# Kernel tuning notes

Hardware: AMD Instinct MI355X
Metric: run time of the kernel (lower is better)

## Reference

```python
import jax, jax.numpy as jnp
import numpy as np

B = 4096      # batch
N = 8192      # feature dim (sorted axis)
K_SPARSE = 512


def setup_inputs() -> dict:
    key = jax.random.key(0)
    x = jax.random.normal(key, (B, N), dtype=jnp.float32)
    return {"x": x, "k": K_SPARSE}


def reference(x, k):
    # Train-phase branch of KSparse.call:
    #   kth_smallest = sort(x)[..., N-1-k]  (the (k+1)-th largest value per row)
    #   out = x * (x > kth_smallest[:, None])
    n = x.shape[-1]
    kth = jnp.sort(x, axis=-1)[..., n - 1 - k]          # [B]
    mask = (x > kth[..., None]).astype(x.dtype)          # strictly greater -> keeps top-k
    return x * mask
```

## Files before the change

kernel.cpp:

```cpp
#include <hip/hip_runtime.h>

#define NTHREADS 512
#define N_FEAT   8192
#define EPT      (N_FEAT / NTHREADS)

__device__ __forceinline__ unsigned f2k(float f) {
    unsigned u = __float_as_uint(f);
    return u ^ (unsigned)(((int)u >> 31) | 0x80000000);
}
__device__ __forceinline__ float k2f(unsigned kk) {
    return __uint_as_float(kk ^ (unsigned)(((int)(~kk) >> 31) | 0x80000000));
}

template<int NB, int SHIFT, bool FILTER>
__device__ __forceinline__ void radix_pass(unsigned* hist, const unsigned (&key)[EPT],
                                           unsigned& prefix, unsigned& pmask, unsigned& r,
                                           unsigned* s_pr, int t) {
    constexpr int PER = NB / 64;
    constexpr int L2P = (PER == 64) ? 6 : 4;
    constexpr int PHYS = NB + 64;

#pragma unroll
    for (int i = 0; i < (PHYS + NTHREADS - 1) / NTHREADS; ++i) {
        int idx = t + i * NTHREADS;
        if (idx < PHYS) hist[idx] = 0;
    }
    __syncthreads();

#pragma unroll
    for (int i = 0; i < EPT; ++i) {
        unsigned kk = key[i];
        if (!FILTER || (kk & pmask) == prefix) {
            unsigned b = (kk >> SHIFT) & (NB - 1);
            atomicAdd(&hist[b + (b >> L2P)], 1u);
        }
    }
    __syncthreads();

    if (t < 64) {
        const unsigned* hbase = hist + t * (PER + 1);
        unsigned C = 0;
#pragma unroll
        for (int j = 0; j < PER; ++j) C += hbase[j];
        unsigned S = C;
#pragma unroll
        for (int off = 1; off < 64; off <<= 1) {
            unsigned v = (unsigned)__shfl_down((int)S, off, 64);
            if (t + off < 64) S += v;
        }
        unsigned carry = S - C;
        if (S >= r && carry < r) {
            unsigned acc = carry;
#pragma unroll
            for (int j = PER - 1; j >= 0; --j) {
                unsigned ge = acc + hbase[j];
                if (ge >= r && acc < r) {
                    s_pr[0] = prefix | ((unsigned)(t * PER + j) << SHIFT);
                    s_pr[1] = r - acc;
                }
                acc = ge;
            }
        }
    }
    __syncthreads();
    prefix = s_pr[0];
    r = s_pr[1];
    pmask |= (unsigned)(NB - 1) << SHIFT;
}

__global__ __launch_bounds__(NTHREADS) void ksparse_kernel(
    const float* __restrict__ x, const int* __restrict__ kptr,
    float* __restrict__ out) {
    const int row = blockIdx.x;
    const int t   = threadIdx.x;
    const size_t base = (size_t)row * N_FEAT;

    __shared__ unsigned hist[4096 + 64];
    __shared__ unsigned s_pr[2];

    const float4* xv = (const float4*)(x + base);
    unsigned key[EPT];
#pragma unroll
    for (int i = 0; i < EPT / 4; ++i) {
        float4 v = xv[t + i * NTHREADS];
        key[4 * i + 0] = f2k(v.x);
        key[4 * i + 1] = f2k(v.y);
        key[4 * i + 2] = f2k(v.z);
        key[4 * i + 3] = f2k(v.w);
    }

    unsigned r = (unsigned)kptr[0] + 1u;
    unsigned prefix = 0, pmask = 0;

    radix_pass<4096, 20, false>(hist, key, prefix, pmask, r, s_pr, t);
    radix_pass<1024, 10, true >(hist, key, prefix, pmask, r, s_pr, t);
    radix_pass<1024,  0, true >(hist, key, prefix, pmask, r, s_pr, t);

    const unsigned kth = prefix;
    float4* ov = (float4*)(out + base);
#pragma unroll
    for (int i = 0; i < EPT / 4; ++i) {
        float4 o;
        unsigned k0 = key[4 * i + 0];
        unsigned k1 = key[4 * i + 1];
        unsigned k2 = key[4 * i + 2];
        unsigned k3 = key[4 * i + 3];
        o.x = (k0 > kth) ? k2f(k0) : 0.0f;
        o.y = (k1 > kth) ? k2f(k1) : 0.0f;
        o.z = (k2 > kth) ? k2f(k2) : 0.0f;
        o.w = (k3 > kth) ? k2f(k3) : 0.0f;
        ov[t + i * NTHREADS] = o;
    }
}

extern "C" void kernel_launch(void* const* d_in, const int* in_sizes, int n_in,
                              void* d_out, int out_size, void* d_ws, size_t ws_size,
                              hipStream_t stream) {
    const float* x = (const float*)d_in[0];
    const int* k   = (const int*)d_in[1];
    float* out     = (float*)d_out;
    const int B = in_sizes[0] / N_FEAT;
    ksparse_kernel<<<B, NTHREADS, 0, stream>>>(x, k, out);
}
```

Before: 63.35 us.

## Replace second and third radix passes with candidate compaction and rank selection

```diff
diff --git a/kernel.cpp b/kernel.cpp
--- a/kernel.cpp
+++ b/kernel.cpp
@@ -3,6 +3,10 @@
 #define NTHREADS 512
 #define N_FEAT   8192
 #define EPT      (N_FEAT / NTHREADS)
+#define NB0      4096
+#define CAP      2048
+
+typedef float f4v __attribute__((ext_vector_type(4)));
 
 __device__ __forceinline__ unsigned f2k(float f) {
     unsigned u = __float_as_uint(f);
@@ -12,104 +16,142 @@
     return __uint_as_float(kk ^ (unsigned)(((int)(~kk) >> 31) | 0x80000000));
 }
 
-template<int NB, int SHIFT, bool FILTER>
-__device__ __forceinline__ void radix_pass(unsigned* hist, const unsigned (&key)[EPT],
-                                           unsigned& prefix, unsigned& pmask, unsigned& r,
-                                           unsigned* s_pr, int t) {
-    constexpr int PER = NB / 64;
-    constexpr int L2P = (PER == 64) ? 6 : 4;
-    constexpr int PHYS = NB + 64;
+__global__ __launch_bounds__(NTHREADS) void ksparse_kernel(
+    const float* __restrict__ x, const int* __restrict__ kptr,
+    float* __restrict__ out) {
+
+    const int t    = threadIdx.x;
+    const int lane = t & 63;
+    const int w    = t >> 6;
+    const size_t base = (size_t)blockIdx.x * N_FEAT;
+
+    __shared__ unsigned hist[NB0];
+    __shared__ unsigned cand[CAP];
+    __shared__ unsigned ws[8];
+    __shared__ unsigned s_bucket, s_r, s_cnt, s_kth;
+
+    const f4v* xv = (const f4v*)(x + base);
+    f4v v0 = xv[t], v1 = xv[t + 512], v2 = xv[t + 1024], v3 = xv[t + 1536];
 
 #pragma unroll
-    for (int i = 0; i < (PHYS + NTHREADS - 1) / NTHREADS; ++i) {
-        int idx = t + i * NTHREADS;
-        if (idx < PHYS) hist[idx] = 0;
+    for (int i = 0; i < NB0 / NTHREADS; ++i) hist[t + i * NTHREADS] = 0u;
+    if (t == 0) s_cnt = 0u;
+    __syncthreads();
+
+    unsigned key[EPT];
+#pragma unroll
+    for (int j = 0; j < 4; ++j) {
+        key[0 + j] = f2k(v0[j]);
+        key[4 + j] = f2k(v1[j]);
+        key[8 + j] = f2k(v2[j]);
+        key[12 + j] = f2k(v3[j]);
+    }
+
+    const unsigned r = (unsigned)kptr[0] + 1u;
+
+#pragma unroll
+    for (int i = 0; i < EPT; ++i) {
+        unsigned b = key[i] >> 20;
+        atomicAdd(&hist[((b & 7u) << 9) | (b >> 3)], 1u);
     }
     __syncthreads();
 
+    unsigned h[8], sum8 = 0;
 #pragma unroll
-    for (int i = 0; i < EPT; ++i) {
-        unsigned kk = key[i];
-        if (!FILTER || (kk & pmask) == prefix) {
-            unsigned b = (kk >> SHIFT) & (NB - 1);
-            atomicAdd(&hist[b + (b >> L2P)], 1u);
+    for (int j = 0; j < 8; ++j) { h[j] = hist[(j << 9) | t]; sum8 += h[j]; }
+    unsigned S = sum8;
+#pragma unroll
+    for (int off = 1; off < 64; off <<= 1) {
+        unsigned q = (unsigned)__shfl_down((int)S, off, 64);
+        if (lane + off < 64) S += q;
+    }
+    if (lane == 0) ws[w] = S;
+    __syncthreads();
+    unsigned above = S - sum8;
+#pragma unroll
+    for (int w2 = 0; w2 < 8; ++w2) if (w2 > w) above += ws[w2];
+    if (above < r && above + sum8 >= r) {
+        unsigned acc = above;
+#pragma unroll
+        for (int j = 7; j >= 0; --j) {
+            if (acc < r && acc + h[j] >= r) { s_bucket = (unsigned)(8 * t + j); s_r = r - acc; }
+            acc += h[j];
         }
     }
     __syncthreads();
+    const unsigned bucket = s_bucket;
+    const unsigned r2 = s_r;
 
-    if (t < 64) {
-        const unsigned* hbase = hist + t * (PER + 1);
-        unsigned C = 0;
 #pragma unroll
-        for (int j = 0; j < PER; ++j) C += hbase[j];
-        unsigned S = C;
-#pragma unroll
-        for (int off = 1; off < 64; off <<= 1) {
-            unsigned v = (unsigned)__shfl_down((int)S, off, 64);
-            if (t + off < 64) S += v;
-        }
-        unsigned carry = S - C;
-        if (S >= r && carry < r) {
-            unsigned acc = carry;
-#pragma unroll
-            for (int j = PER - 1; j >= 0; --j) {
-                unsigned ge = acc + hbase[j];
-                if (ge >= r && acc < r) {
-                    s_pr[0] = prefix | ((unsigned)(t * PER + j) << SHIFT);
-                    s_pr[1] = r - acc;
-                }
-                acc = ge;
-            }
+    for (int i = 0; i < EPT; ++i) {
+        if ((key[i] >> 20) == bucket) {
+            unsigned p = atomicAdd(&s_cnt, 1u);
+            if (p < CAP) cand[p] = key[i];
         }
     }
     __syncthreads();
-    prefix = s_pr[0];
-    r = s_pr[1];
-    pmask |= (unsigned)(NB - 1) << SHIFT;
-}
+    const unsigned m = s_cnt;
 
-__global__ __launch_bounds__(NTHREADS) void ksparse_kernel(
-    const float* __restrict__ x, const int* __restrict__ kptr,
-    float* __restrict__ out) {
-    const int row = blockIdx.x;
-    const int t   = threadIdx.x;
-    const size_t base = (size_t)row * N_FEAT;
+    if (m <= CAP) {
+        for (unsigned i = t; i < m; i += NTHREADS) {
+            unsigned ki = cand[i], g = 0, ge = 0;
+            for (unsigned j = 0; j < m; ++j) {
+                unsigned kj = cand[j];
+                g  += (kj > ki);
+                ge += (kj >= ki);
+            }
+            if (g < r2 && ge >= r2) s_kth = ki;
+        }
+    } else {
+        unsigned prefix = bucket << 20;
+        unsigned rr = r2;
+        for (int pass = 0; pass < 2; ++pass) {
+            const int shift = (pass == 0) ? 10 : 0;
+            const unsigned hm = (pass == 0) ? 0xFFF00000u : 0xFFFFFC00u;
+            hist[t] = 0u; hist[t + 512] = 0u;
+            __syncthreads();
+            for (int i = 0; i < EPT; ++i)
+                if ((key[i] & hm) == prefix)
+                    atomicAdd(&hist[(key[i] >> shift) & 1023u], 1u);
+            __syncthreads();
+            if (t < 64) {
+                const unsigned* hb = hist + t * 16;
+                unsigned C = 0;
+                for (int j2 = 0; j2 < 16; ++j2) C += hb[j2];
+                unsigned S2 = C;
+                for (int off = 1; off < 64; off <<= 1) {
+                    unsigned q = (unsigned)__shfl_down((int)S2, off, 64);
+                    if (lane + off < 64) S2 += q;
+                }
+                unsigned carry = S2 - C;
+                if (S2 >= rr && carry < rr) {
+                    unsigned acc = carry;
+                    for (int j2 = 15; j2 >= 0; --j2) {
+                        unsigned ge2 = acc + hb[j2];
+                        if (acc < rr && ge2 >= rr) { s_bucket = (unsigned)(t * 16 + j2); s_r = rr - acc; }
+                        acc = ge2;
+                    }
+                }
+            }
+            __syncthreads();
+            prefix |= s_bucket << shift;
+            rr = s_r;
+        }
+        if (t == 0) s_kth = prefix;
+    }
+    __syncthreads();
+    const unsigned kth = s_kth;
 
-    __shared__ unsigned hist[4096 + 64];
-    __shared__ unsigned s_pr[2];
-
-    const float4* xv = (const float4*)(x + base);
-    unsigned key[EPT];
+    f4v* ov = (f4v*)(out + base);
 #pragma unroll
-    for (int i = 0; i < EPT / 4; ++i) {
-        float4 v = xv[t + i * NTHREADS];
-        key[4 * i + 0] = f2k(v.x);
-        key[4 * i + 1] = f2k(v.y);
-        key[4 * i + 2] = f2k(v.z);
-        key[4 * i + 3] = f2k(v.w);
-    }
-
-    unsigned r = (unsigned)kptr[0] + 1u;
-    unsigned prefix = 0, pmask = 0;
-
-    radix_pass<4096, 20, false>(hist, key, prefix, pmask, r, s_pr, t);
-    radix_pass<1024, 10, true >(hist, key, prefix, pmask, r, s_pr, t);
-    radix_pass<1024,  0, true >(hist, key, prefix, pmask, r, s_pr, t);
-
-    const unsigned kth = prefix;
-    float4* ov = (float4*)(out + base);
+    for (int i = 0; i < 4; ++i) {
+        f4v o;
 #pragma unroll
-    for (int i = 0; i < EPT / 4; ++i) {
-        float4 o;
-        unsigned k0 = key[4 * i + 0];
-        unsigned k1 = key[4 * i + 1];
-        unsigned k2 = key[4 * i + 2];
-        unsigned k3 = key[4 * i + 3];
-        o.x = (k0 > kth) ? k2f(k0) : 0.0f;
-        o.y = (k1 > kth) ? k2f(k1) : 0.0f;
-        o.z = (k2 > kth) ? k2f(k2) : 0.0f;
-        o.w = (k3 > kth) ? k2f(k3) : 0.0f;
-        ov[t + i * NTHREADS] = o;
+        for (int j = 0; j < 4; ++j) {
+            unsigned kk = key[4 * i + j];
+            o[j] = (kk > kth) ? k2f(kk) : 0.0f;
+        }
+        __builtin_nontemporal_store(o, ov + t + i * NTHREADS);
     }
 }
 
```

Result: faster. 52.32 us (-17.4%).

## Process two rows per block with 256-thread groups and 11/11/10 radix passes

Applied to the files above, without the earlier changes.

```diff
diff --git a/kernel.cpp b/kernel.cpp
--- a/kernel.cpp
+++ b/kernel.cpp
@@ -1,8 +1,15 @@
 #include <hip/hip_runtime.h>
 
 #define NTHREADS 512
+#define GT       256
+#define NGRP     (NTHREADS / GT)
 #define N_FEAT   8192
-#define EPT      (N_FEAT / NTHREADS)
+#define VPT      8
+#define NB1      2048
+#define SKSZ     (NB1 + NB1 / 8)
+#define SK(b)    ((b) + ((b) >> 3))
+
+typedef float f4v __attribute__((ext_vector_type(4)));
 
 __device__ __forceinline__ unsigned f2k(float f) {
     unsigned u = __float_as_uint(f);
@@ -12,104 +19,123 @@
     return __uint_as_float(kk ^ (unsigned)(((int)(~kk) >> 31) | 0x80000000));
 }
 
-template<int NB, int SHIFT, bool FILTER>
-__device__ __forceinline__ void radix_pass(unsigned* hist, const unsigned (&key)[EPT],
-                                           unsigned& prefix, unsigned& pmask, unsigned& r,
-                                           unsigned* s_pr, int t) {
-    constexpr int PER = NB / 64;
-    constexpr int L2P = (PER == 64) ? 6 : 4;
-    constexpr int PHYS = NB + 64;
-
+template<int PER>
+__device__ __forceinline__ void scan_locate(unsigned* __restrict__ histg,
+                                            volatile unsigned* wsg,
+                                            unsigned* s_bucket, unsigned* s_r,
+                                            unsigned r, int tg, int lane, int wg) {
+    unsigned h[PER], sum = 0;
 #pragma unroll
-    for (int i = 0; i < (PHYS + NTHREADS - 1) / NTHREADS; ++i) {
-        int idx = t + i * NTHREADS;
-        if (idx < PHYS) hist[idx] = 0;
+    for (int j = 0; j < PER; ++j) {
+        const int b = PER * tg + j;
+        h[j] = histg[SK(b)];
+        histg[SK(b)] = 0u;
+        sum += h[j];
     }
+    unsigned S = sum;
+#pragma unroll
+    for (int off = 1; off < 64; off <<= 1) {
+        unsigned q = (unsigned)__shfl_down((int)S, off, 64);
+        if (lane + off < 64) S += q;
+    }
+    if (lane == 0) wsg[wg] = S;
     __syncthreads();
-
+    unsigned above = S - sum;
 #pragma unroll
-    for (int i = 0; i < EPT; ++i) {
-        unsigned kk = key[i];
-        if (!FILTER || (kk & pmask) == prefix) {
-            unsigned b = (kk >> SHIFT) & (NB - 1);
-            atomicAdd(&hist[b + (b >> L2P)], 1u);
+    for (int w2 = 1; w2 < GT / 64; ++w2) if (w2 > wg) above += wsg[w2];
+    if (above < r && above + sum >= r) {
+        unsigned acc = above;
+#pragma unroll
+        for (int j = PER - 1; j >= 0; --j) {
+            if (acc < r && acc + h[j] >= r) { *s_bucket = (unsigned)(PER * tg + j); *s_r = r - acc; }
+            acc += h[j];
         }
     }
     __syncthreads();
-
-    if (t < 64) {
-        const unsigned* hbase = hist + t * (PER + 1);
-        unsigned C = 0;
-#pragma unroll
-        for (int j = 0; j < PER; ++j) C += hbase[j];
-        unsigned S = C;
-#pragma unroll
-        for (int off = 1; off < 64; off <<= 1) {
-            unsigned v = (unsigned)__shfl_down((int)S, off, 64);
-            if (t + off < 64) S += v;
-        }
-        unsigned carry = S - C;
-        if (S >= r && carry < r) {
-            unsigned acc = carry;
-#pragma unroll
-            for (int j = PER - 1; j >= 0; --j) {
-                unsigned ge = acc + hbase[j];
-                if (ge >= r && acc < r) {
-                    s_pr[0] = prefix | ((unsigned)(t * PER + j) << SHIFT);
-                    s_pr[1] = r - acc;
-                }
-                acc = ge;
-            }
-        }
-    }
-    __syncthreads();
-    prefix = s_pr[0];
-    r = s_pr[1];
-    pmask |= (unsigned)(NB - 1) << SHIFT;
 }
 
 __global__ __launch_bounds__(NTHREADS) void ksparse_kernel(
     const float* __restrict__ x, const int* __restrict__ kptr,
-    float* __restrict__ out) {
-    const int row = blockIdx.x;
-    const int t   = threadIdx.x;
-    const size_t base = (size_t)row * N_FEAT;
+    float* __restrict__ out, int nrows) {
 
-    __shared__ unsigned hist[4096 + 64];
-    __shared__ unsigned s_pr[2];
+    const int t    = threadIdx.x;
+    const int g    = t >> 8;
+    const int tg   = t & (GT - 1);
+    const int lane = t & 63;
+    const int wg   = (t >> 6) & 3;
 
-    const float4* xv = (const float4*)(x + base);
-    unsigned key[EPT];
+    __shared__ unsigned hist[NGRP][SKSZ];
+    __shared__ unsigned ws[NGRP][GT / 64];
+    __shared__ unsigned s_bucket[NGRP], s_r[NGRP];
+
+    const int rowid = blockIdx.x * NGRP + g;
+    const bool valid = rowid < nrows;
+    const size_t base = (size_t)(valid ? rowid : 0) * N_FEAT;
+    const f4v* xv = (const f4v*)(x + base);
+
+    f4v v[VPT];
 #pragma unroll
-    for (int i = 0; i < EPT / 4; ++i) {
-        float4 v = xv[t + i * NTHREADS];
-        key[4 * i + 0] = f2k(v.x);
-        key[4 * i + 1] = f2k(v.y);
-        key[4 * i + 2] = f2k(v.z);
-        key[4 * i + 3] = f2k(v.w);
-    }
+    for (int i = 0; i < VPT; ++i) v[i] = xv[tg + i * GT];
+
+#pragma unroll
+    for (int i = 0; i < (NGRP * SKSZ) / NTHREADS; ++i)
+        (&hist[0][0])[t + i * NTHREADS] = 0u;
+    __syncthreads();
+
+    unsigned key[VPT][4];
+#pragma unroll
+    for (int i = 0; i < VPT; ++i)
+#pragma unroll
+        for (int j = 0; j < 4; ++j) key[i][j] = f2k(v[i][j]);
 
     unsigned r = (unsigned)kptr[0] + 1u;
-    unsigned prefix = 0, pmask = 0;
+    unsigned* histg = hist[g];
 
-    radix_pass<4096, 20, false>(hist, key, prefix, pmask, r, s_pr, t);
-    radix_pass<1024, 10, true >(hist, key, prefix, pmask, r, s_pr, t);
-    radix_pass<1024,  0, true >(hist, key, prefix, pmask, r, s_pr, t);
+#pragma unroll
+    for (int i = 0; i < VPT; ++i)
+#pragma unroll
+        for (int j = 0; j < 4; ++j)
+            atomicAdd(&histg[SK(key[i][j] >> 21)], 1u);
+    __syncthreads();
+    scan_locate<NB1 / GT>(histg, ws[g], &s_bucket[g], &s_r[g], r, tg, lane, wg);
+    const unsigned b1 = s_bucket[g];
+    r = s_r[g];
 
-    const unsigned kth = prefix;
-    float4* ov = (float4*)(out + base);
 #pragma unroll
-    for (int i = 0; i < EPT / 4; ++i) {
-        float4 o;
-        unsigned k0 = key[4 * i + 0];
-        unsigned k1 = key[4 * i + 1];
-        unsigned k2 = key[4 * i + 2];
-        unsigned k3 = key[4 * i + 3];
-        o.x = (k0 > kth) ? k2f(k0) : 0.0f;
-        o.y = (k1 > kth) ? k2f(k1) : 0.0f;
-        o.z = (k2 > kth) ? k2f(k2) : 0.0f;
-        o.w = (k3 > kth) ? k2f(k3) : 0.0f;
-        ov[t + i * NTHREADS] = o;
+    for (int i = 0; i < VPT; ++i)
+#pragma unroll
+        for (int j = 0; j < 4; ++j) {
+            unsigned kk = key[i][j];
+            if ((kk >> 21) == b1) atomicAdd(&histg[SK((kk >> 10) & 2047u)], 1u);
+        }
+    __syncthreads();
+    scan_locate<NB1 / GT>(histg, ws[g], &s_bucket[g], &s_r[g], r, tg, lane, wg);
+    const unsigned p22 = (b1 << 11) | s_bucket[g];
+    r = s_r[g];
+
+#pragma unroll
+    for (int i = 0; i < VPT; ++i)
+#pragma unroll
+        for (int j = 0; j < 4; ++j) {
+            unsigned kk = key[i][j];
+            if ((kk >> 10) == p22) atomicAdd(&histg[SK(kk & 1023u)], 1u);
+        }
+    __syncthreads();
+    scan_locate<1024 / GT>(histg, ws[g], &s_bucket[g], &s_r[g], r, tg, lane, wg);
+    const unsigned kth = (p22 << 10) | s_bucket[g];
+
+    if (valid) {
+        f4v* ov = (f4v*)(out + base);
+#pragma unroll
+        for (int i = 0; i < VPT; ++i) {
+            f4v o;
+#pragma unroll
+            for (int j = 0; j < 4; ++j) {
+                unsigned kk = key[i][j];
+                o[j] = (kk > kth) ? k2f(kk) : 0.0f;
+            }
+            __builtin_nontemporal_store(o, ov + tg + i * GT);
+        }
     }
 }
 
@@ -120,5 +146,6 @@
     const int* k   = (const int*)d_in[1];
     float* out     = (float*)d_out;
     const int B = in_sizes[0] / N_FEAT;
-    ksparse_kernel<<<B, NTHREADS, 0, stream>>>(x, k, out);
+    const int grid = (B + NGRP - 1) / NGRP;
+    ksparse_kernel<<<grid, NTHREADS, 0, stream>>>(x, k, out, B);
 }
```

Measured after the change: 55.77 us. 1.14x faster.
